# Kernel optimization log

Measured on AMD Instinct MI355X. Metric: run time of the kernel, lower is better.

The kernel has to match this reference:

```python
import jax, jax.numpy as jnp
import numpy as np

TIMESTEPS = 100  # init kwarg: timesteps
CLIP_MAX = 1e10


def setup_inputs() -> dict:
    key = jax.random.key(0)
    kR, kT, krho, kb = jax.random.split(key, 4)
    N, M, C = 1024, 64, 4
    R = jax.random.uniform(kR, (N, M, M), dtype=jnp.float32)
    R = R / jnp.sum(R, axis=2, keepdims=True)   # row-stochastic mobility matrices
    T = jax.random.uniform(kT, (N, C, C), dtype=jnp.float32)
    T = T / jnp.sum(T, axis=2, keepdims=True)   # row-stochastic compartment transitions
    rho0 = jax.random.uniform(krho, (N, M, C), dtype=jnp.float32) * 0.01
    beta = jax.random.uniform(kb, (N,), dtype=jnp.float32) * 0.2
    return {"R": R, "T": T, "rho0": rho0, "beta": beta}


def _infect_prob(neff, ntot, beta):
    # py0-style contact infection: infectious compartment index 1
    ninf = neff[..., 1]                                    # (N, M, M)
    x = beta[:, None, None] * ninf / ntot[:, None, :]      # (N, M, M)
    return 1.0 - jnp.exp(jnp.sum(jnp.log(1.0 - x), axis=2))  # (N, M)


def reference(R, T, rho0, beta):
    N, M, C = rho0.shape
    # ntot is loop-invariant (same math as recomputing per step)
    ntot = jnp.sum(R, axis=1)                              # (N, M)
    # faithful to tf.reshape(tf.transpose(R), (-1, M, M, 1)): full-reverse transpose then reshape
    Rt = jnp.transpose(R).reshape(N, M, M, 1)
    e0 = jnp.zeros((C,), rho0.dtype).at[0].set(1.0)        # one-hot: new infections -> compartment 0

    def step(rho, _):
        neff = rho.reshape(N, M, 1, C) * Rt                # (N, M, M, C)
        p = _infect_prob(neff, ntot, beta)                 # (N, M)
        new_inf = (1.0 - jnp.sum(rho, axis=-1)) * jnp.einsum('ijk,ik->ij', R, p)
        rho_new = jnp.einsum('ijk,ikl->ijl', rho, T) + new_inf[:, :, None] * e0
        rho_new = jnp.clip(rho_new, 0.0, CLIP_MAX)
        return rho_new, rho                                # trajectory records pre-update state

    _, trajs = jax.lax.scan(step, rho0, None, length=TIMESTEPS)
    return trajs                                           # (timesteps, N, M, C)
```

## Files before the change

### kernel.cpp

```cpp
#include <hip/hip_runtime.h>

typedef __attribute__((ext_vector_type(2))) float f32x2;

#define NS 1024
#define MM 64
#define CC 4
#define NSTEPS 100
#define CLIPMAX 1e10f

__device__ __forceinline__ float rdlane(float v, int k) {
    return __uint_as_float(__builtin_amdgcn_readlane(__float_as_uint(v), k));
}
__device__ __forceinline__ float sfirst(float v) {
    return __uint_as_float(__builtin_amdgcn_readfirstlane(__float_as_uint(v)));
}

extern "C" __global__
__attribute__((amdgpu_flat_work_group_size(64, 64), amdgpu_waves_per_eu(1, 1)))
void metapop_kernel(
    const float* __restrict__ R,
    const float* __restrict__ T,
    const float* __restrict__ rho0,
    const float* __restrict__ beta,
    float* __restrict__ out)
{
    const int n    = blockIdx.x;
    const int lane = threadIdx.x;

    __shared__ float pbuf[MM];

    const float* Rn = R + (size_t)n * (MM * MM);

    f32x2 Rrow2[32];
    {
        const float4* p4 = (const float4*)(Rn + lane * MM);
        #pragma unroll
        for (int q = 0; q < 16; ++q) {
            float4 v = p4[q];
            Rrow2[2*q]   = (f32x2){v.x, v.y};
            Rrow2[2*q+1] = (f32x2){v.z, v.w};
        }
    }

    float nt = 0.f;
    #pragma unroll
    for (int i = 0; i < MM; ++i) nt += Rn[i * MM + lane];
    const float binv = beta[n] / nt;

    float S1 = 0.f, S2 = 0.f, S3 = 0.f, S4 = 0.f;
    {
        const int q     = n >> 4;
        const int a     = ((n & 15) << 2) + (lane >> 4);
        const int sbase = (lane & 15) << 6;
        #pragma unroll
        for (int j = 0; j < MM; ++j) {
            float g  = R[(size_t)(sbase + j) * (MM * MM) + a * MM + q]
                     * rdlane(binv, j);
            float g2 = g * g;
            S1 += g;  S2 += g2;  S3 += g2 * g;  S4 += g2 * g2;
        }
    }
    const float c1 = S1, c2 = 0.5f * S2, c3 = (1.f / 3.f) * S3, c4 = 0.25f * S4;
    const float c1sq = c1 * c1;
    const float d1 = c1;
    const float d2 = c2 - 0.5f * c1sq;
    const float d3 = c3 - c1 * c2 + (1.f / 6.f) * c1sq * c1;
    const float d4 = c4 - c1 * c3 - 0.5f * c2 * c2 + 0.5f * c1sq * c2
                   - (1.f / 24.f) * c1sq * c1sq;

    #pragma unroll
    for (int q = 0; q < 32; ++q) asm volatile("" : "+v"(Rrow2[q]));

    float tt[CC][CC];
    {
        const float* Tn = T + n * (CC * CC);
        #pragma unroll
        for (int k = 0; k < CC; ++k)
            #pragma unroll
            for (int l = 0; l < CC; ++l)
                tt[k][l] = sfirst(Tn[k * CC + l]);
    }

    float rh[CC];
    {
        float4 v = *(const float4*)(rho0 + (size_t)n * (MM * CC) + lane * CC);
        rh[0] = v.x; rh[1] = v.y; rh[2] = v.z; rh[3] = v.w;
    }

    float* ob = out + (size_t)n * (MM * CC) + lane * CC;
    const size_t stride = (size_t)NS * MM * CC;

    for (int step = 0; step < NSTEPS; ++step) {
        *(float4*)(ob + (size_t)step * stride) =
            make_float4(rh[0], rh[1], rh[2], rh[3]);

        const float r1 = rh[1];
        const float p  = r1 * (d1 + r1 * (d2 + r1 * (d3 + r1 * d4)));

        pbuf[lane] = p;

        f32x2 a0 = {0.f, 0.f}, a1 = {0.f, 0.f}, a2 = {0.f, 0.f}, a3 = {0.f, 0.f};
        {
            const float4* pb4 = (const float4*)pbuf;
            #pragma unroll
            for (int q = 0; q < 4; ++q) {
                float4 pv;
                pv = pb4[q];
                a0 += Rrow2[2*q]      * (f32x2){pv.x, pv.y};
                a0 += Rrow2[2*q + 1]  * (f32x2){pv.z, pv.w};
                pv = pb4[q + 4];
                a1 += Rrow2[2*q + 8]  * (f32x2){pv.x, pv.y};
                a1 += Rrow2[2*q + 9]  * (f32x2){pv.z, pv.w};
                pv = pb4[q + 8];
                a2 += Rrow2[2*q + 16] * (f32x2){pv.x, pv.y};
                a2 += Rrow2[2*q + 17] * (f32x2){pv.z, pv.w};
                pv = pb4[q + 12];
                a3 += Rrow2[2*q + 24] * (f32x2){pv.x, pv.y};
                a3 += Rrow2[2*q + 25] * (f32x2){pv.z, pv.w};
            }
        }
        const f32x2 aa = (a0 + a1) + (a2 + a3);
        const float ssum = aa.x + aa.y;
        const float sr   = (rh[0] + rh[1]) + (rh[2] + rh[3]);
        const float ninf = (1.f - sr) * ssum;

        float nr[CC];
        #pragma unroll
        for (int l = 0; l < CC; ++l) {
            float v = rh[0] * tt[0][l] + rh[1] * tt[1][l]
                    + rh[2] * tt[2][l] + rh[3] * tt[3][l];
            if (l == 0) v += ninf;
            nr[l] = fminf(fmaxf(v, 0.f), CLIPMAX);
        }
        #pragma unroll
        for (int l = 0; l < CC; ++l) rh[l] = nr[l];
    }
}

extern "C" void kernel_launch(void* const* d_in, const int* in_sizes, int n_in,
                              void* d_out, int out_size, void* d_ws, size_t ws_size,
                              hipStream_t stream) {
    const float* R    = (const float*)d_in[0];
    const float* T    = (const float*)d_in[1];
    const float* rho0 = (const float*)d_in[2];
    const float* beta = (const float*)d_in[3];
    float* out = (float*)d_out;
    hipLaunchKernelGGL(metapop_kernel, dim3(NS), dim3(64), 0, stream,
                       R, T, rho0, beta, out);
}
```

Baseline: 55.31 us.

## Pre-transpose R into workspace so cumulant gather reads are coalesced

Adds a separate transpose kernel that rewrites R into a workspace layout matching the scattered reverse-transpose access of the main kernel. The main kernel's cumulant loop then reads contiguous per-lane values instead of strided global gathers. This costs an extra kernel launch plus a full read and scattered write of R (16 MB), trading uncoalesced reads in the main kernel for an extra pass over memory.

```diff
diff --git a/kernel.cpp b/kernel.cpp
--- a/kernel.cpp
+++ b/kernel.cpp
@@ -15,6 +15,25 @@
     return __uint_as_float(__builtin_amdgcn_readfirstlane(__float_as_uint(v)));
 }
 
+extern "C" __global__ __launch_bounds__(256)
+void transpose_kernel(const float* __restrict__ R, float* __restrict__ ws) {
+    const int s = blockIdx.x;
+    const int t = threadIdx.x;
+    const float* Rs = R + (size_t)s * (MM * MM);
+    const int j   = s & 63;
+    const int shi = s >> 6;
+    #pragma unroll
+    for (int k = 0; k < 16; ++k) {
+        const int flat = t + 256 * k;
+        const int m = flat >> 6;
+        const int q = flat & 63;
+        const float v = Rs[flat];
+        const int n = (q << 4) | (m >> 2);
+        const int i = ((m & 3) << 4) | shi;
+        ws[(size_t)n * (MM * MM) + j * MM + i] = v;
+    }
+}
+
 extern "C" __global__
 __attribute__((amdgpu_flat_work_group_size(64, 64), amdgpu_waves_per_eu(1, 1)))
 void metapop_kernel(
@@ -22,6 +41,7 @@
     const float* __restrict__ T,
     const float* __restrict__ rho0,
     const float* __restrict__ beta,
+    const float* __restrict__ ws,
     float* __restrict__ out)
 {
     const int n    = blockIdx.x;
@@ -49,13 +69,10 @@
 
     float S1 = 0.f, S2 = 0.f, S3 = 0.f, S4 = 0.f;
     {
-        const int q     = n >> 4;
-        const int a     = ((n & 15) << 2) + (lane >> 4);
-        const int sbase = (lane & 15) << 6;
+        const float* wsn = ws + (size_t)n * (MM * MM);
         #pragma unroll
         for (int j = 0; j < MM; ++j) {
-            float g  = R[(size_t)(sbase + j) * (MM * MM) + a * MM + q]
-                     * rdlane(binv, j);
+            float g  = wsn[j * MM + lane] * rdlane(binv, j);
             float g2 = g * g;
             S1 += g;  S2 += g2;  S3 += g2 * g;  S4 += g2 * g2;
         }
@@ -145,6 +162,9 @@
     const float* rho0 = (const float*)d_in[2];
     const float* beta = (const float*)d_in[3];
     float* out = (float*)d_out;
+    float* ws  = (float*)d_ws;
+
+    hipLaunchKernelGGL(transpose_kernel, dim3(NS), dim3(256), 0, stream, R, ws);
     hipLaunchKernelGGL(metapop_kernel, dim3(NS), dim3(64), 0, stream,
-                       R, T, rho0, beta, out);
+                       R, T, rho0, beta, ws, out);
 }
```

After: 61.35 us. 1.11x slower.
